# Performance work log

Hardware: AMD Instinct MI355X
Metric: run time of the kernel (lower is better)

The kernel has to match this reference:

```python
import jax, jax.numpy as jnp
import numpy as np

K = 1024
D = 256
BETA = 0.25


def setup_inputs() -> dict:
    key = jax.random.key(0)
    kx, kc = jax.random.split(key)
    x = jax.random.normal(kx, (64, 32, 32, D), dtype=jnp.float32)
    limit = 1.0 / K
    codebook = jax.random.uniform(kc, (K, D), dtype=jnp.float32, minval=-limit, maxval=limit)
    return {"x": x, "codebook": codebook}


def reference(x, codebook):
    flat = x.reshape(-1, D)                                   # [N, D]
    x2 = jnp.sum(jnp.square(flat), axis=1, keepdims=True)     # [N, 1]
    e2 = jnp.sum(jnp.square(codebook), axis=1)                # [K]
    sim = flat @ codebook.T                                   # [N, K]
    dist = x2 + e2 - 2.0 * sim                                # [N, K]
    idx = jnp.argmin(dist, axis=1)                            # [N]
    q = codebook[idx].reshape(x.shape)                        # [..., D]

    q_st = jax.lax.stop_gradient(q)
    x_st = jax.lax.stop_gradient(x)
    commit = jnp.mean(jnp.square(q_st - x))
    codebk = jnp.mean(jnp.square(q - x_st))
    loss = BETA * commit + codebk

    # code-usage statistics via histogram (equivalent to mean of one-hot)
    counts = jnp.zeros((K,), dtype=x.dtype).at[idx].add(1.0)
    probs = counts / flat.shape[0]
    eps = jnp.asarray(1e-10, dtype=x.dtype)
    H = -jnp.sum(probs * jnp.log2(probs + eps))               # bits/index
    perplexity = jnp.exp(H * jnp.log(jnp.asarray(2.0, dtype=x.dtype)))
    usage = jnp.sum((probs > 0).astype(x.dtype)) / float(K)

    y = x + jax.lax.stop_gradient(q - x)                      # straight-through
    return y, idx, loss, perplexity, usage, H
```

## Files before the change

### kernel.cpp

```cpp
#include <hip/hip_runtime.h>
#include <math.h>

#define D       256
#define KCODES  1024
#define NROWS   65536
#define BETA    0.25f
#define MARGIN  1e-3f
#define MAXSURV 7

typedef __attribute__((ext_vector_type(8))) short bf16x8;
typedef __attribute__((ext_vector_type(4))) float f32x4;

__device__ __forceinline__ unsigned int bf16_rne(float f) {
    unsigned int u = __float_as_uint(f);
    return (u + 0x7FFFu + ((u >> 16) & 1u)) >> 16;
}
__device__ __forceinline__ f32x4 mfma16(bf16x8 a, bf16x8 b, f32x4 c) {
    return __builtin_amdgcn_mfma_f32_16x16x32_bf16(a, b, c, 0, 0, 0);
}

__global__ __launch_bounds__(256) void split_cb_kernel(const float* __restrict__ cb,
                                                       ushort* __restrict__ cs,
                                                       float* __restrict__ e2f) {
    int code = blockIdx.x * 4 + (threadIdx.x >> 6);
    int lane = threadIdx.x & 63;
    float4 v = ((const float4*)(cb + (size_t)code * D))[lane];
    double s = (double)v.x * v.x + (double)v.y * v.y +
               (double)v.z * v.z + (double)v.w * v.w;
    ushort* ph = cs + (size_t)code * 256 + lane * 4;
    ph[0] = (ushort)bf16_rne(v.x); ph[1] = (ushort)bf16_rne(v.y);
    ph[2] = (ushort)bf16_rne(v.z); ph[3] = (ushort)bf16_rne(v.w);
    #pragma unroll
    for (int off = 32; off > 0; off >>= 1) s += __shfl_down(s, off, 64);
    if (lane == 0) e2f[code] = (float)s;
}

__global__ __launch_bounds__(512, 4) void screen_kernel(
    const float* __restrict__ x, const ushort* __restrict__ cs,
    const float* __restrict__ e2f, const float* __restrict__ cb,
    float* __restrict__ out_idxf, unsigned int* __restrict__ counts,
    float* __restrict__ y, float* __restrict__ msepart)
{
    __shared__ __attribute__((aligned(16))) ushort Bt[2][32 * 256];
    __shared__ unsigned mrg[128 * 33];
    __shared__ float x2s[128];
    #define MRG(r, j) mrg[(r) * 33 + (j)]

    const int tid  = threadIdx.x;
    const int wave = tid >> 6, lane = tid & 63;
    const int quad = lane >> 4, m = lane & 15;
    const int rowBase = blockIdx.x * 128;
    const int wrb = rowBase + wave * 16;

    const int sc = tid & 31, sp = tid >> 5;
    const int swW = (sc & 7) << 4;
    const int wb0 = (sc * 512 + sp * 32) ^ swW;
    const int wb1 = (sc * 512 + sp * 32 + 16) ^ swW;
    bf16x8 stg[2];
    {
        const ushort* src = cs + (size_t)sc * 256 + sp * 16;
        stg[0] = *(const bf16x8*)&src[0];
        stg[1] = *(const bf16x8*)&src[8];
    }

    bf16x8 af[8];
    {
        const float* xr = x + (size_t)(wrb + m) * D;
        double s = 0.0;
        #pragma unroll
        for (int c = 0; c < 8; ++c) {
            float4 f0 = *(const float4*)&xr[c * 32 + quad * 8];
            float4 f1 = *(const float4*)&xr[c * 32 + quad * 8 + 4];
            s += (double)f0.x * f0.x + (double)f0.y * f0.y +
                 (double)f0.z * f0.z + (double)f0.w * f0.w;
            s += (double)f1.x * f1.x + (double)f1.y * f1.y +
                 (double)f1.z * f1.z + (double)f1.w * f1.w;
            float ff[8] = {f0.x, f0.y, f0.z, f0.w, f1.x, f1.y, f1.z, f1.w};
            #pragma unroll
            for (int j = 0; j < 8; ++j) af[c][j] = (short)bf16_rne(ff[j]);
        }
        s += __shfl_xor(s, 16, 64);
        s += __shfl_xor(s, 32, 64);
        if (quad == 0) x2s[wave * 16 + m] = (float)s;
    }

    unsigned u1[4], u2[4];
    #pragma unroll
    for (int r = 0; r < 4; ++r) { u1[r] = 0xFFFFFFFFu; u2[r] = 0xFFFFFFFFu; }

    const int swR = (m & 7) << 4;

    for (int kt = 0; kt < KCODES / 32; ++kt) {
        {
            char* dstb = (char*)&Bt[kt & 1][0];
            *(bf16x8*)(dstb + wb0) = stg[0];
            *(bf16x8*)(dstb + wb1) = stg[1];
        }
        __syncthreads();
        if (kt < KCODES / 32 - 1) {
            const ushort* src = cs + (size_t)((kt + 1) * 32 + sc) * 256 + sp * 16;
            stg[0] = *(const bf16x8*)&src[0];
            stg[1] = *(const bf16x8*)&src[8];
        }

        float e2pa = e2f[kt * 32 + m] + 0.5f;
        float e2pb = e2f[kt * 32 + 16 + m] + 0.5f;

        const char* Bcur = (const char*)&Bt[kt & 1][0];
        #pragma unroll
        for (int nt = 0; nt < 2; ++nt) {
            f32x4 acc = {0.f, 0.f, 0.f, 0.f};
            const int base = (nt * 16 + m) * 512 + quad * 16;
            __builtin_amdgcn_s_setprio(1);
            #pragma unroll
            for (int c = 0; c < 8; ++c) {
                bf16x8 bh = *(const bf16x8*)(Bcur + ((base + c * 64) ^ swR));
                acc = mfma16(af[c], bh, acc);
            }
            __builtin_amdgcn_s_setprio(0);
            unsigned kcode = kt * 32 + nt * 16 + m;
            float e2p = nt ? e2pb : e2pa;
            #pragma unroll
            for (int r = 0; r < 4; ++r) {
                float d = fmaf(-2.f, acc[r], e2p);
                unsigned u = (__float_as_uint(d) & 0xFFFFFC00u) | kcode;
                u2[r] = min(max(u, u1[r]), u2[r]);
                u1[r] = min(u, u1[r]);
            }
        }
    }

    #pragma unroll
    for (int r = 0; r < 4; ++r) {
        int rowloc = wave * 16 + quad * 4 + r;
        MRG(rowloc, m * 2 + 0) = u1[r];
        MRG(rowloc, m * 2 + 1) = u2[r];
    }
    __syncthreads();
    if (tid < 128) {
        unsigned umin = 0xFFFFFFFFu;
        #pragma unroll
        for (int j = 0; j < 32; ++j) umin = min(umin, MRG(tid, j));
        float dfloor = __uint_as_float(umin & 0xFFFFFC00u);
        unsigned limu = (__float_as_uint(dfloor + MARGIN) & 0xFFFFFC00u) | 1023u;
        ushort out[8] = {0, 0, 0, 0, 0, 0, 0, 0};
        int cnt = 0;
        for (int j = 0; j < 32; ++j) {
            unsigned u = MRG(tid, j);
            if (u <= limu && cnt < MAXSURV) { out[1 + cnt] = (ushort)(u & 1023u); ++cnt; }
        }
        out[0] = (ushort)cnt;
        *(bf16x8*)&mrg[tid * 33] = *(bf16x8*)out;
    }
    __syncthreads();

    #pragma unroll 2
    for (int i = 0; i < 16; ++i) {
        int rl  = wave * 16 + i;
        int row = rowBase + rl;
        const ushort* lst = (const ushort*)&mrg[rl * 33];
        int cnt = lst[0];
        float4 xv = ((const float4*)(x + (size_t)row * D))[lane];

        int bk;
        if (cnt == 1) {
            bk = lst[1];
        } else {
            float x2 = x2s[rl];
            float bestd = 1e30f;
            int   bestk = 0;
            for (int s = 0; s < cnt; ++s) {
                int k = lst[1 + s];
                float4 cv = ((const float4*)(cb + (size_t)k * D))[lane];
                double p = (double)xv.x * cv.x + (double)xv.y * cv.y +
                           (double)xv.z * cv.z + (double)xv.w * cv.w;
                #pragma unroll
                for (int off = 32; off > 0; off >>= 1) p += __shfl_down(p, off, 64);
                float simf = (float)p;
                float tt   = x2 + e2f[k];
                float dq   = tt - 2.0f * simf;
                if (dq < bestd || (dq == bestd && k < bestk)) { bestd = dq; bestk = k; }
            }
            bk = __shfl(bestk, 0, 64);
        }
        if (lane == 0) {
            out_idxf[row] = (float)bk;
            atomicAdd(&counts[bk], 1u);
        }
        float4 q = ((const float4*)(cb + (size_t)bk * D))[lane];
        float4 dv;
        dv.x = q.x - xv.x; dv.y = q.y - xv.y; dv.z = q.z - xv.z; dv.w = q.w - xv.w;
        float4 yv;
        yv.x = xv.x + dv.x; yv.y = xv.y + dv.y; yv.z = xv.z + dv.z; yv.w = xv.w + dv.w;
        ((float4*)(y + (size_t)row * D))[lane] = yv;
        float s = dv.x * dv.x + dv.y * dv.y + dv.z * dv.z + dv.w * dv.w;
        #pragma unroll
        for (int off = 32; off > 0; off >>= 1) s += __shfl_down(s, off, 64);
        if (lane == 0) msepart[row] = s;
    }
    #undef MRG
}

__global__ __launch_bounds__(1024) void stats_kernel(
    const unsigned int* __restrict__ counts, const float* __restrict__ msepart,
    float* __restrict__ outs)
{
    int t = threadIdx.x;
    float ms = 0.f;
    #pragma unroll
    for (int j = 0; j < 64; ++j) ms += msepart[t + 1024 * j];

    float p = (float)counts[t] * (1.0f / 65536.0f);
    float h = -p * log2f(p + 1e-10f);
    float u = (p > 0.f) ? 1.f : 0.f;
    #pragma unroll
    for (int off = 32; off > 0; off >>= 1) {
        h  += __shfl_down(h,  off, 64);
        u  += __shfl_down(u,  off, 64);
        ms += __shfl_down(ms, off, 64);
    }
    __shared__ float hs[16], us[16], mss[16];
    int lane = t & 63, w = t >> 6;
    if (lane == 0) { hs[w] = h; us[w] = u; mss[w] = ms; }
    __syncthreads();
    if (t == 0) {
        float H = 0.f, U = 0.f, M = 0.f;
        #pragma unroll
        for (int i = 0; i < 16; ++i) { H += hs[i]; U += us[i]; M += mss[i]; }
        float m = M * (1.0f / 16777216.0f);
        float loss = BETA * m + m;
        float perp = expf(H * 0.69314718055994530942f);
        outs[0] = loss;
        outs[1] = perp;
        outs[2] = U * (1.0f / 1024.0f);
        outs[3] = H;
    }
}

extern "C" void kernel_launch(void* const* d_in, const int* in_sizes, int n_in,
                              void* d_out, int out_size, void* d_ws, size_t ws_size,
                              hipStream_t stream) {
    const float* x  = (const float*)d_in[0];
    const float* cb = (const float*)d_in[1];
    float* out      = (float*)d_out;

    float* y        = out;
    float* out_idxf = out + 16777216;
    float* outs     = out + 16777216 + 65536;

    float*        e2f     = (float*)((char*)d_ws + 262144);
    unsigned int* counts  = (unsigned int*)((char*)d_ws + 266240);
    ushort*       cs      = (ushort*)((char*)d_ws + 1318976);
    float*        msepart = (float*)((char*)d_ws + 1843264);

    hipMemsetAsync((char*)d_ws + 266240, 0, 4096, stream);
    split_cb_kernel<<<KCODES / 4, 256, 0, stream>>>(cb, cs, e2f);
    screen_kernel<<<NROWS / 128, 512, 0, stream>>>(x, cs, e2f, cb,
                                                   out_idxf, counts, y, msepart);
    stats_kernel<<<1, 1024, 0, stream>>>(counts, msepart, outs);
}
```

Before: 193.0 us.

## Screen codebook distances with int8 MFMA and widen exact-rescore margin

Replaces the bf16 screening GEMM with int8 MFMA. The codebook is quantized with a fixed scale and each x row with a per-row absmax scale, so K=256 takes four 16x16x64 int8 MFMAs instead of eight bf16 ones, and the LDS tile is half the size with padding in place of the XOR swizzle. To absorb the larger quantization error, the margin and survivor cap are raised, and the top candidate is always kept for exact fp64 rescoring. It also folds the counts memset into split_cb_kernel. The risks are more rescoring work and wrong indices if int8 error exceeds the margin.

```diff
diff --git a/kernel.cpp b/kernel.cpp
--- a/kernel.cpp
+++ b/kernel.cpp
@@ -5,45 +5,53 @@
 #define KCODES  1024
 #define NROWS   65536
 #define BETA    0.25f
-#define MARGIN  1e-3f
-#define MAXSURV 7
+#define MARGIN  3e-3f
+#define MAXSURV 15
 
 typedef __attribute__((ext_vector_type(8))) short bf16x8;
 typedef __attribute__((ext_vector_type(4))) float f32x4;
-
-__device__ __forceinline__ unsigned int bf16_rne(float f) {
-    unsigned int u = __float_as_uint(f);
-    return (u + 0x7FFFu + ((u >> 16) & 1u)) >> 16;
-}
-__device__ __forceinline__ f32x4 mfma16(bf16x8 a, bf16x8 b, f32x4 c) {
-    return __builtin_amdgcn_mfma_f32_16x16x32_bf16(a, b, c, 0, 0, 0);
+typedef __attribute__((ext_vector_type(4))) int   i32x4;
+
+__device__ __forceinline__ i32x4 mfma_i8(i32x4 a, i32x4 b, i32x4 c) {
+    return __builtin_amdgcn_mfma_i32_16x16x64_i8(a, b, c, 0, 0, 0);
+}
+__device__ __forceinline__ int pack4(int a, int b, int c, int d) {
+    return (a & 255) | ((b & 255) << 8) | ((c & 255) << 16) | (d << 24);
 }
 
 __global__ __launch_bounds__(256) void split_cb_kernel(const float* __restrict__ cb,
-                                                       ushort* __restrict__ cs,
-                                                       float* __restrict__ e2f) {
+                                                       unsigned char* __restrict__ cs8,
+                                                       float* __restrict__ e2f,
+                                                       unsigned int* __restrict__ counts) {
+    if (threadIdx.x < 4) counts[blockIdx.x * 4 + threadIdx.x] = 0u;
     int code = blockIdx.x * 4 + (threadIdx.x >> 6);
     int lane = threadIdx.x & 63;
     float4 v = ((const float4*)(cb + (size_t)code * D))[lane];
     double s = (double)v.x * v.x + (double)v.y * v.y +
                (double)v.z * v.z + (double)v.w * v.w;
-    ushort* ph = cs + (size_t)code * 256 + lane * 4;
-    ph[0] = (ushort)bf16_rne(v.x); ph[1] = (ushort)bf16_rne(v.y);
-    ph[2] = (ushort)bf16_rne(v.z); ph[3] = (ushort)bf16_rne(v.w);
+    int q0 = __float2int_rn(v.x * 130048.0f);
+    int q1 = __float2int_rn(v.y * 130048.0f);
+    int q2 = __float2int_rn(v.z * 130048.0f);
+    int q3 = __float2int_rn(v.w * 130048.0f);
+    int d0 = lane * 4;
+    int cp = d0 >> 5, qq = (d0 >> 3) & 3, j0 = d0 & 7;
+    int p  = (cp >> 1) * 64 + qq * 16 + (cp & 1) * 8 + j0;
+    *(int*)&cs8[(size_t)code * 256 + p] = pack4(q0, q1, q2, q3);
     #pragma unroll
     for (int off = 32; off > 0; off >>= 1) s += __shfl_down(s, off, 64);
     if (lane == 0) e2f[code] = (float)s;
 }
 
 __global__ __launch_bounds__(512, 4) void screen_kernel(
-    const float* __restrict__ x, const ushort* __restrict__ cs,
+    const float* __restrict__ x, const unsigned char* __restrict__ cs8,
     const float* __restrict__ e2f, const float* __restrict__ cb,
     float* __restrict__ out_idxf, unsigned int* __restrict__ counts,
     float* __restrict__ y, float* __restrict__ msepart)
 {
-    __shared__ __attribute__((aligned(16))) ushort Bt[2][32 * 256];
+    __shared__ __attribute__((aligned(16))) char Bt[2][32 * 272];
     __shared__ unsigned mrg[128 * 33];
     __shared__ float x2s[128];
+    __shared__ float sxn[128];
     #define MRG(r, j) mrg[(r) * 33 + (j)]
 
     const int tid  = threadIdx.x;
@@ -53,76 +61,89 @@
     const int wrb = rowBase + wave * 16;
 
     const int sc = tid & 31, sp = tid >> 5;
-    const int swW = (sc & 7) << 4;
-    const int wb0 = (sc * 512 + sp * 32) ^ swW;
-    const int wb1 = (sc * 512 + sp * 32 + 16) ^ swW;
-    bf16x8 stg[2];
-    {
-        const ushort* src = cs + (size_t)sc * 256 + sp * 16;
-        stg[0] = *(const bf16x8*)&src[0];
-        stg[1] = *(const bf16x8*)&src[8];
-    }
-
-    bf16x8 af[8];
-    {
-        const float* xr = x + (size_t)(wrb + m) * D;
-        double s = 0.0;
-        #pragma unroll
-        for (int c = 0; c < 8; ++c) {
-            float4 f0 = *(const float4*)&xr[c * 32 + quad * 8];
-            float4 f1 = *(const float4*)&xr[c * 32 + quad * 8 + 4];
-            s += (double)f0.x * f0.x + (double)f0.y * f0.y +
-                 (double)f0.z * f0.z + (double)f0.w * f0.w;
-            s += (double)f1.x * f1.x + (double)f1.y * f1.y +
-                 (double)f1.z * f1.z + (double)f1.w * f1.w;
-            float ff[8] = {f0.x, f0.y, f0.z, f0.w, f1.x, f1.y, f1.z, f1.w};
-            #pragma unroll
-            for (int j = 0; j < 8; ++j) af[c][j] = (short)bf16_rne(ff[j]);
-        }
-        s += __shfl_xor(s, 16, 64);
-        s += __shfl_xor(s, 32, 64);
-        if (quad == 0) x2s[wave * 16 + m] = (float)s;
+    i32x4 stg;
+    stg = *(const i32x4*)&cs8[(size_t)sc * 256 + sp * 16];
+
+    const float* xr = x + (size_t)(wrb + m) * D;
+    double s = 0.0;
+    float amax = 0.0f;
+    #pragma unroll
+    for (int c = 0; c < 8; ++c) {
+        float4 f0 = *(const float4*)&xr[c * 32 + quad * 8];
+        float4 f1 = *(const float4*)&xr[c * 32 + quad * 8 + 4];
+        s += (double)f0.x * f0.x + (double)f0.y * f0.y +
+             (double)f0.z * f0.z + (double)f0.w * f0.w;
+        s += (double)f1.x * f1.x + (double)f1.y * f1.y +
+             (double)f1.z * f1.z + (double)f1.w * f1.w;
+        amax = fmaxf(amax, fmaxf(fmaxf(fabsf(f0.x), fabsf(f0.y)),
+                                 fmaxf(fabsf(f0.z), fabsf(f0.w))));
+        amax = fmaxf(amax, fmaxf(fmaxf(fabsf(f1.x), fabsf(f1.y)),
+                                 fmaxf(fabsf(f1.z), fabsf(f1.w))));
+    }
+    s += __shfl_xor(s, 16, 64);
+    s += __shfl_xor(s, 32, 64);
+    amax = fmaxf(amax, __shfl_xor(amax, 16, 64));
+    amax = fmaxf(amax, __shfl_xor(amax, 32, 64));
+    float rmax = fmaxf(amax, 1e-20f);
+    float inv  = 127.0f / rmax;
+    if (quad == 0) {
+        x2s[wave * 16 + m] = (float)s;
+        sxn[wave * 16 + m] = -2.0f * (rmax * (1.0f / 127.0f)) * (1.0f / 130048.0f);
+    }
+
+    i32x4 af[4];
+    #pragma unroll
+    for (int ck = 0; ck < 4; ++ck) {
+        float4 a0 = *(const float4*)&xr[(2 * ck) * 32 + quad * 8];
+        float4 a1 = *(const float4*)&xr[(2 * ck) * 32 + quad * 8 + 4];
+        float4 b0 = *(const float4*)&xr[(2 * ck + 1) * 32 + quad * 8];
+        float4 b1 = *(const float4*)&xr[(2 * ck + 1) * 32 + quad * 8 + 4];
+        af[ck][0] = pack4(__float2int_rn(a0.x * inv), __float2int_rn(a0.y * inv),
+                          __float2int_rn(a0.z * inv), __float2int_rn(a0.w * inv));
+        af[ck][1] = pack4(__float2int_rn(a1.x * inv), __float2int_rn(a1.y * inv),
+                          __float2int_rn(a1.z * inv), __float2int_rn(a1.w * inv));
+        af[ck][2] = pack4(__float2int_rn(b0.x * inv), __float2int_rn(b0.y * inv),
+                          __float2int_rn(b0.z * inv), __float2int_rn(b0.w * inv));
+        af[ck][3] = pack4(__float2int_rn(b1.x * inv), __float2int_rn(b1.y * inv),
+                          __float2int_rn(b1.z * inv), __float2int_rn(b1.w * inv));
     }
 
     unsigned u1[4], u2[4];
     #pragma unroll
     for (int r = 0; r < 4; ++r) { u1[r] = 0xFFFFFFFFu; u2[r] = 0xFFFFFFFFu; }
 
-    const int swR = (m & 7) << 4;
+    *(i32x4*)&Bt[0][sc * 272 + sp * 16] = stg;
+    __syncthreads();
+    float sxr[4];
+    #pragma unroll
+    for (int r = 0; r < 4; ++r) sxr[r] = sxn[wave * 16 + quad * 4 + r];
 
     for (int kt = 0; kt < KCODES / 32; ++kt) {
-        {
-            char* dstb = (char*)&Bt[kt & 1][0];
-            *(bf16x8*)(dstb + wb0) = stg[0];
-            *(bf16x8*)(dstb + wb1) = stg[1];
-        }
-        __syncthreads();
-        if (kt < KCODES / 32 - 1) {
-            const ushort* src = cs + (size_t)((kt + 1) * 32 + sc) * 256 + sp * 16;
-            stg[0] = *(const bf16x8*)&src[0];
-            stg[1] = *(const bf16x8*)&src[8];
-        }
+        if (kt > 0) {
+            *(i32x4*)&Bt[kt & 1][sc * 272 + sp * 16] = stg;
+            __syncthreads();
+        }
+        if (kt < KCODES / 32 - 1)
+            stg = *(const i32x4*)&cs8[(size_t)((kt + 1) * 32 + sc) * 256 + sp * 16];
 
         float e2pa = e2f[kt * 32 + m] + 0.5f;
         float e2pb = e2f[kt * 32 + 16 + m] + 0.5f;
 
-        const char* Bcur = (const char*)&Bt[kt & 1][0];
+        const char* Bcur = &Bt[kt & 1][0];
         #pragma unroll
         for (int nt = 0; nt < 2; ++nt) {
-            f32x4 acc = {0.f, 0.f, 0.f, 0.f};
-            const int base = (nt * 16 + m) * 512 + quad * 16;
+            i32x4 acc = {0, 0, 0, 0};
+            const char* bp = Bcur + (nt * 16 + m) * 272 + quad * 16;
             __builtin_amdgcn_s_setprio(1);
             #pragma unroll
-            for (int c = 0; c < 8; ++c) {
-                bf16x8 bh = *(const bf16x8*)(Bcur + ((base + c * 64) ^ swR));
-                acc = mfma16(af[c], bh, acc);
-            }
+            for (int ck = 0; ck < 4; ++ck)
+                acc = mfma_i8(af[ck], *(const i32x4*)(bp + ck * 64), acc);
             __builtin_amdgcn_s_setprio(0);
             unsigned kcode = kt * 32 + nt * 16 + m;
             float e2p = nt ? e2pb : e2pa;
             #pragma unroll
             for (int r = 0; r < 4; ++r) {
-                float d = fmaf(-2.f, acc[r], e2p);
+                float d = fmaf(sxr[r], (float)acc[r], e2p);
                 unsigned u = (__float_as_uint(d) & 0xFFFFFC00u) | kcode;
                 u2[r] = min(max(u, u1[r]), u2[r]);
                 u1[r] = min(u, u1[r]);
@@ -143,14 +164,20 @@
         for (int j = 0; j < 32; ++j) umin = min(umin, MRG(tid, j));
         float dfloor = __uint_as_float(umin & 0xFFFFFC00u);
         unsigned limu = (__float_as_uint(dfloor + MARGIN) & 0xFFFFFC00u) | 1023u;
-        ushort out[8] = {0, 0, 0, 0, 0, 0, 0, 0};
-        int cnt = 0;
+        ushort out[16];
+        #pragma unroll
+        for (int j = 0; j < 16; ++j) out[j] = 0;
+        out[1] = (ushort)(umin & 1023u);
+        int cnt = 1;
         for (int j = 0; j < 32; ++j) {
             unsigned u = MRG(tid, j);
-            if (u <= limu && cnt < MAXSURV) { out[1 + cnt] = (ushort)(u & 1023u); ++cnt; }
+            if (u <= limu && u != umin && cnt < MAXSURV) {
+                out[1 + cnt] = (ushort)(u & 1023u); ++cnt;
+            }
         }
         out[0] = (ushort)cnt;
-        *(bf16x8*)&mrg[tid * 33] = *(bf16x8*)out;
+        *(bf16x8*)&mrg[tid * 33]     = *(bf16x8*)&out[0];
+        *(bf16x8*)&mrg[tid * 33 + 4] = *(bf16x8*)&out[8];
     }
     __syncthreads();
 
@@ -169,8 +196,8 @@
             float x2 = x2s[rl];
             float bestd = 1e30f;
             int   bestk = 0;
-            for (int s = 0; s < cnt; ++s) {
-                int k = lst[1 + s];
+            for (int ss = 0; ss < cnt; ++ss) {
+                int k = lst[1 + ss];
                 float4 cv = ((const float4*)(cb + (size_t)k * D))[lane];
                 double p = (double)xv.x * cv.x + (double)xv.y * cv.y +
                            (double)xv.z * cv.z + (double)xv.w * cv.w;
@@ -193,10 +220,10 @@
         float4 yv;
         yv.x = xv.x + dv.x; yv.y = xv.y + dv.y; yv.z = xv.z + dv.z; yv.w = xv.w + dv.w;
         ((float4*)(y + (size_t)row * D))[lane] = yv;
-        float s = dv.x * dv.x + dv.y * dv.y + dv.z * dv.z + dv.w * dv.w;
-        #pragma unroll
-        for (int off = 32; off > 0; off >>= 1) s += __shfl_down(s, off, 64);
-        if (lane == 0) msepart[row] = s;
+        float s2 = dv.x * dv.x + dv.y * dv.y + dv.z * dv.z + dv.w * dv.w;
+        #pragma unroll
+        for (int off = 32; off > 0; off >>= 1) s2 += __shfl_down(s2, off, 64);
+        if (lane == 0) msepart[row] = s2;
     }
     #undef MRG
 }
@@ -248,14 +275,13 @@
     float* out_idxf = out + 16777216;
     float* outs     = out + 16777216 + 65536;
 
-    float*        e2f     = (float*)((char*)d_ws + 262144);
-    unsigned int* counts  = (unsigned int*)((char*)d_ws + 266240);
-    ushort*       cs      = (ushort*)((char*)d_ws + 1318976);
-    float*        msepart = (float*)((char*)d_ws + 1843264);
-
-    hipMemsetAsync((char*)d_ws + 266240, 0, 4096, stream);
-    split_cb_kernel<<<KCODES / 4, 256, 0, stream>>>(cb, cs, e2f);
-    screen_kernel<<<NROWS / 128, 512, 0, stream>>>(x, cs, e2f, cb,
+    float*         e2f     = (float*)((char*)d_ws + 262144);
+    unsigned int*  counts  = (unsigned int*)((char*)d_ws + 266240);
+    unsigned char* cs8     = (unsigned char*)((char*)d_ws + 1318976);
+    float*         msepart = (float*)((char*)d_ws + 1843264);
+
+    split_cb_kernel<<<KCODES / 4, 256, 0, stream>>>(cb, cs8, e2f, counts);
+    screen_kernel<<<NROWS / 128, 512, 0, stream>>>(x, cs8, e2f, cb,
                                                    out_idxf, counts, y, msepart);
     stats_kernel<<<1, 1024, 0, stream>>>(counts, msepart, outs);
 }
```

After: 198.8 us. 3.0% more time.
